# Optimization experiments

Measured on AMD Instinct MI355X. Metric: run time of the kernel, lower is better.

## Reference

```python
import jax, jax.numpy as jnp
import numpy as np

N_NODES = 100000
N_EDGES = 3200000
N_FEAT = 128
H = 16
N_CLASSES = 10


def gcn_conv(x, edge_index, W, b, num_nodes):
    """PyG GCNConv (eval): add self-loops, symmetric norm, linear, scatter-add, bias."""
    xw = x @ W  # [N, out]
    loops = jnp.arange(num_nodes, dtype=edge_index.dtype)
    src = jnp.concatenate([edge_index[0], loops])  # message sources (x_j)
    dst = jnp.concatenate([edge_index[1], loops])  # aggregation targets
    ones = jnp.ones(src.shape[0], dtype=xw.dtype)
    deg = jax.ops.segment_sum(ones, dst, num_segments=num_nodes)
    dinv = jnp.where(deg > 0, jax.lax.rsqrt(deg), 0.0)
    norm = dinv[src] * dinv[dst]  # [E+N]
    msg = xw[src] * norm[:, None]  # gather + scale
    out = jax.ops.segment_sum(msg, dst, num_segments=num_nodes)
    return out + b


def setup_inputs() -> dict:
    key = jax.random.key(0)
    ks = jax.random.split(key, 8)
    x = jax.random.normal(ks[0], (N_NODES, N_FEAT), dtype=jnp.float32)
    edge_index = jax.random.randint(ks[1], (2, N_EDGES), 0, N_NODES, dtype=jnp.int64)
    topo_edges = jax.random.randint(ks[2], (2, N_EDGES), 0, N_NODES, dtype=jnp.int64)
    s1 = 1.0 / np.sqrt(N_FEAT)
    s4 = 1.0 / np.sqrt(2 * H)
    W1 = jax.random.normal(ks[3], (N_FEAT, H), dtype=jnp.float32) * s1
    b1 = jnp.zeros((H,), dtype=jnp.float32)
    W2 = jax.random.normal(ks[4], (N_FEAT, H), dtype=jnp.float32) * s1
    b2 = jnp.zeros((H,), dtype=jnp.float32)
    W4 = jax.random.normal(ks[5], (2 * H, N_CLASSES), dtype=jnp.float32) * s4
    b4 = jnp.zeros((N_CLASSES,), dtype=jnp.float32)
    return {"x": x, "edge_index": edge_index, "topo_edges": topo_edges,
            "W1": W1, "b1": b1, "W2": W2, "b2": b2, "W4": W4, "b4": b4}


def reference(x, edge_index, topo_edges, W1, b1, W2, b2, W4, b4):
    n = x.shape[0]
    # branch 1: structural edges
    x1 = jax.nn.relu(gcn_conv(x, edge_index, W1, b1, n))
    # branch 2: topological edges
    x2 = jax.nn.relu(gcn_conv(x, topo_edges, W2, b2, n))
    # dropout is identity in eval mode
    h = jnp.concatenate([x1, x2], axis=1)  # [N, 2H]
    logits = gcn_conv(h, edge_index, W4, b4, n)  # [N, num_classes]
    return jax.nn.log_softmax(logits, axis=1)
```

## Files before the change

### kernel.cpp

```cpp
#include <hip/hip_runtime.h>
#include <hip/hip_fp16.h>

#define N_NODES 100000
#define N_EDGES 3200000
#define NB 1024
#define BW 98
#define SLOT 4096


__global__ void k_zero(int* __restrict__ bcur1, int* __restrict__ bcur2) {
    int i = blockIdx.x * blockDim.x + threadIdx.x;
    if (i < NB) { bcur1[i] = 0; bcur2[i] = 0; }
}

__global__ __launch_bounds__(256) void k_part(const int* __restrict__ ei, const int* __restrict__ te,
                                              int* __restrict__ bcur1, int* __restrict__ bcur2,
                                              unsigned* __restrict__ tmp1, unsigned* __restrict__ tmp2,
                                              int E, int PB) {
    __shared__ int h[NB];
    __shared__ int bas[NB];
    int gb = blockIdx.x;
    bool g2 = gb >= PB;
    const int* ed = g2 ? te : ei;
    int* bcur     = g2 ? bcur2 : bcur1;
    unsigned* tmp = g2 ? tmp2 : tmp1;
    int blk = g2 ? gb - PB : gb;
    int t = threadIdx.x;
    for (int i = t; i < NB; i += 256) h[i] = 0;
    __syncthreads();
    int base = blk * 8192, end = min(base + 8192, E);
    for (int e = base + t; e < end; e += 256) atomicAdd(&h[ed[E + e] / BW], 1);
    __syncthreads();
    for (int i = t; i < NB; i += 256) {
        int c = h[i];
        bas[i] = c ? atomicAdd(&bcur[i], c) : 0;
    }
    __syncthreads();
    for (int i = t; i < NB; i += 256) h[i] = 0;
    __syncthreads();
    for (int e = base + t; e < end; e += 256) {
        int d = ed[E + e], s = ed[e];
        int b = d / BW;
        int r = bas[b] + atomicAdd(&h[b], 1);
        if (r < SLOT) tmp[(size_t)b * SLOT + r] = ((unsigned)(d - b * BW) << 20) | (unsigned)s;
    }
}

__global__ __launch_bounds__(256) void k_csr(const int* __restrict__ bcur1, const int* __restrict__ bcur2,
                                             unsigned* __restrict__ tmp1, unsigned* __restrict__ tmp2,
                                             int2* __restrict__ pk1, int2* __restrict__ pk2,
                                             float* __restrict__ dinv1, float* __restrict__ dinv2, int n) {
    __shared__ unsigned stage[SLOT];
    __shared__ int ncnt[BW], noff[BW], nrank[BW];
    int gb = blockIdx.x;
    bool g2 = gb >= NB;
    int b = g2 ? gb - NB : gb;
    unsigned* tmp = g2 ? tmp2 : tmp1;
    int2* pk      = g2 ? pk2 : pk1;
    float* dinv   = g2 ? dinv2 : dinv1;
    int sz = min((g2 ? bcur2 : bcur1)[b], SLOT);
    int t = threadIdx.x;
    if (t < BW) { ncnt[t] = 0; nrank[t] = 0; }
    __syncthreads();
    size_t base = (size_t)b * SLOT;
    for (int i = t; i < sz; i += 256) {
        unsigned v = tmp[base + i];
        stage[i] = v;
        atomicAdd(&ncnt[v >> 20], 1);
    }
    __syncthreads();
    if (t == 0) {
        int run = 0;
        for (int k = 0; k < BW; ++k) { noff[k] = run; run += ncnt[k]; }
    }
    __syncthreads();
    int nd = b * BW + t;
    if (t < BW && nd < n) {
        pk[nd] = make_int2((int)base + noff[t], ncnt[t]);
        dinv[nd] = rsqrtf((float)ncnt[t] + 1.f);
    }
    for (int i = t; i < sz; i += 256) {
        unsigned v = stage[i];
        int ld = v >> 20;
        int r = atomicAdd(&nrank[ld], 1);
        tmp[base + noff[ld] + r] = v & 0xFFFFFu;
    }
}

__global__ __launch_bounds__(256) void k_gemm12(
    const float* __restrict__ x,
    const float* __restrict__ W1, const float* __restrict__ W2,
    const float* __restrict__ dinv1, const float* __restrict__ dinv2,
    __half* __restrict__ xwh1, __half* __restrict__ xwh2, int n) {
    __shared__ float Wl[128][32];
    __shared__ float xs[8][128];
    int t = threadIdx.x;
    for (int i = t; i < 128 * 16; i += 256) {
        int k = i / 16, o = i % 16;
        Wl[k][o]      = W1[i];
        Wl[k][o + 16] = W2[i];
    }
    int node0 = blockIdx.x * 8;
    for (int i = t; i < 8 * 128; i += 256) {
        int r = i >> 7, c = i & 127;
        int node = node0 + r;
        xs[r][c] = (node < n) ? x[node * 128 + c] : 0.f;
    }
    __syncthreads();
    int r = t >> 5, o = t & 31;
    int node = node0 + r;
    if (node < n) {
        float s = 0.f;
        #pragma unroll
        for (int k = 0; k < 128; ++k) s += xs[r][k] * Wl[k][o];
        if (o < 16) xwh1[(size_t)node * 16 + o]        = __float2half(s * dinv1[node]);
        else        xwh2[(size_t)node * 16 + (o - 16)] = __float2half(s * dinv2[node]);
    }
}

__global__ __launch_bounds__(256) void k_gather12(
    const __half* __restrict__ xwh1, const __half* __restrict__ xwh2,
    const unsigned* __restrict__ csr1, const unsigned* __restrict__ csr2,
    const int2* __restrict__ pk1, const int2* __restrict__ pk2,
    const float* __restrict__ dinv1, const float* __restrict__ dinv2,
    const float* __restrict__ b1, const float* __restrict__ b2,
    __half* __restrict__ h, int n) {
    int t = threadIdx.x;
    int node = blockIdx.x * 8 + (t >> 5);
    int c = t & 31;
    if (node >= n) return;
    bool g1 = (c < 16);
    int cl = g1 ? c : (c - 16);
    const __half* xw    = g1 ? xwh1 : xwh2;
    const unsigned* csr = g1 ? csr1 : csr2;
    int2 oc = g1 ? pk1[node] : pk2[node];
    int o = oc.x, m = oc.y;
    float di = g1 ? dinv1[node] : dinv2[node];
    float acc = __half2float(xw[(size_t)node * 16 + cl]);
    int k = 0;
    for (; k + 4 <= m; k += 4) {
        unsigned j0 = csr[o + k], j1 = csr[o + k + 1], j2 = csr[o + k + 2], j3 = csr[o + k + 3];
        acc += __half2float(xw[(size_t)j0 * 16 + cl]);
        acc += __half2float(xw[(size_t)j1 * 16 + cl]);
        acc += __half2float(xw[(size_t)j2 * 16 + cl]);
        acc += __half2float(xw[(size_t)j3 * 16 + cl]);
    }
    for (; k < m; ++k) acc += __half2float(xw[(size_t)csr[o + k] * 16 + cl]);
    acc *= di;
    float bv = g1 ? b1[cl] : b2[cl];
    float v = acc + bv;
    h[(size_t)node * 32 + c] = __float2half(v > 0.f ? v : 0.f);
}

__global__ void k_gemm3(const __half* __restrict__ h, const float* __restrict__ W4,
                        const float* __restrict__ dinv1, __half* __restrict__ zsh, int n) {
    int i = blockIdx.x * blockDim.x + threadIdx.x;
    if (i >= n) return;
    float hr[32];
    const __half2* hp = (const __half2*)(h + (size_t)i * 32);
    #pragma unroll
    for (int q = 0; q < 16; ++q) {
        float2 f = __half22float2(hp[q]);
        hr[2 * q] = f.x; hr[2 * q + 1] = f.y;
    }
    float di = dinv1[i];
    #pragma unroll
    for (int c = 0; c < 10; ++c) {
        float s = 0.f;
        #pragma unroll
        for (int k = 0; k < 32; ++k) s += hr[k] * W4[k * 10 + c];
        zsh[(size_t)i * 16 + c] = __float2half(s * di);
    }
}

__global__ __launch_bounds__(256) void k_gather3(
    const __half* __restrict__ zsh,
    const unsigned* __restrict__ csr1, const int2* __restrict__ pk1,
    const float* __restrict__ dinv1,
    const float* __restrict__ b4, float* __restrict__ out, int n) {
    int t = threadIdx.x;
    int node = blockIdx.x * 16 + (t >> 4);
    int c = t & 15;
    if (node >= n) return;
    bool act = (c < 10);
    int cc = act ? c : 0;
    float di = dinv1[node];
    float acc = __half2float(zsh[(size_t)node * 16 + cc]);
    int2 oc = pk1[node];
    int o = oc.x, m = oc.y;
    int k = 0;
    for (; k + 4 <= m; k += 4) {
        unsigned j0 = csr1[o + k], j1 = csr1[o + k + 1], j2 = csr1[o + k + 2], j3 = csr1[o + k + 3];
        acc += __half2float(zsh[(size_t)j0 * 16 + cc]);
        acc += __half2float(zsh[(size_t)j1 * 16 + cc]);
        acc += __half2float(zsh[(size_t)j2 * 16 + cc]);
        acc += __half2float(zsh[(size_t)j3 * 16 + cc]);
    }
    for (; k < m; ++k) acc += __half2float(zsh[(size_t)csr1[o + k] * 16 + cc]);
    float logit = acc * di + b4[cc];
    float mv = act ? logit : -1e30f;
    #pragma unroll
    for (int w = 8; w >= 1; w >>= 1) mv = fmaxf(mv, __shfl_xor(mv, w, 16));
    float ex = act ? expf(logit - mv) : 0.f;
    float ssum = ex;
    #pragma unroll
    for (int w = 8; w >= 1; w >>= 1) ssum += __shfl_xor(ssum, w, 16);
    if (act) out[(size_t)node * 10 + c] = logit - mv - logf(ssum);
}

extern "C" void kernel_launch(void* const* d_in, const int* in_sizes, int n_in,
                              void* d_out, int out_size, void* d_ws, size_t ws_size,
                              hipStream_t stream) {
    const float* x  = (const float*)d_in[0];
    const int*   ei = (const int*)d_in[1];
    const int*   te = (const int*)d_in[2];
    const float* W1 = (const float*)d_in[3];
    const float* b1 = (const float*)d_in[4];
    const float* W2 = (const float*)d_in[5];
    const float* b2 = (const float*)d_in[6];
    const float* W4 = (const float*)d_in[7];
    const float* b4 = (const float*)d_in[8];
    float* out = (float*)d_out;

    const int N = N_NODES, E = N_EDGES;

    char* w = (char*)d_ws;
    auto alloc = [&](size_t bytes) { void* p = (void*)w; w += (bytes + 255) & ~255ull; return p; };
    int*      bcur1 = (int*)alloc((size_t)NB * 4);
    int*      bcur2 = (int*)alloc((size_t)NB * 4);
    int2*     pk1   = (int2*)alloc((size_t)N * 8);
    int2*     pk2   = (int2*)alloc((size_t)N * 8);
    float*    dinv1 = (float*)alloc((size_t)N * 4);
    float*    dinv2 = (float*)alloc((size_t)N * 4);
    unsigned* tmp1  = (unsigned*)alloc((size_t)NB * SLOT * 4);
    unsigned* tmp2  = (unsigned*)alloc((size_t)NB * SLOT * 4);
    __half*   xwh1  = (__half*)alloc((size_t)N * 16 * 2);
    __half*   xwh2  = (__half*)alloc((size_t)N * 16 * 2);
    __half*   h     = (__half*)alloc((size_t)N * 32 * 2);
    __half*   zsh   = (__half*)alloc((size_t)N * 16 * 2);

    const int PB = (E + 8191) / 8192;
    k_zero<<<(NB + 255) / 256, 256, 0, stream>>>(bcur1, bcur2);
    k_part<<<2 * PB, 256, 0, stream>>>(ei, te, bcur1, bcur2, tmp1, tmp2, E, PB);
    k_csr<<<2 * NB, 256, 0, stream>>>(bcur1, bcur2, tmp1, tmp2, pk1, pk2, dinv1, dinv2, N);
    k_gemm12<<<(N + 7) / 8, 256, 0, stream>>>(x, W1, W2, dinv1, dinv2, xwh1, xwh2, N);
    k_gather12<<<(N + 7) / 8, 256, 0, stream>>>(xwh1, xwh2, tmp1, tmp2, pk1, pk2,
                                                dinv1, dinv2, b1, b2, h, N);
    k_gemm3<<<(N + 255) / 256, 256, 0, stream>>>(h, W4, dinv1, zsh, N);
    k_gather3<<<(N + 15) / 16, 256, 0, stream>>>(zsh, tmp1, pk1, dinv1, b4, out, N);
}
```

Measured before the change: 461.5 us.

## Locally sort edge chunk in LDS before scattering to bucket slots

The partition kernel now counting-sorts each chunk of edges by destination bucket in shared memory, using a block-wide prefix scan, and then writes them to global bucket slots in sorted order. Consecutive threads therefore write to contiguous addresses instead of scattering randomly. The chunk size doubles to 16384 edges per block, so each block needs about 77 KB of dynamic LDS. In exchange there are fewer blocks and lower occupancy, and every output element pays for a binary search over the bucket offsets.

```diff
diff --git a/kernel.cpp b/kernel.cpp
--- a/kernel.cpp
+++ b/kernel.cpp
@@ -6,6 +6,7 @@
 #define NB 1024
 #define BW 98
 #define SLOT 4096
+#define CHUNK 16384
 
 
 __global__ void k_zero(int* __restrict__ bcur1, int* __restrict__ bcur2) {
@@ -17,8 +18,13 @@
                                               int* __restrict__ bcur1, int* __restrict__ bcur2,
                                               unsigned* __restrict__ tmp1, unsigned* __restrict__ tmp2,
                                               int E, int PB) {
-    __shared__ int h[NB];
-    __shared__ int bas[NB];
+    extern __shared__ unsigned smem[];
+    unsigned* sorted = smem;
+    int* loff = (int*)(smem + CHUNK);
+    int* rank = loff + NB;
+    int* bas  = rank + NB;
+    int* ps   = bas + NB;
+
     int gb = blockIdx.x;
     bool g2 = gb >= PB;
     const int* ed = g2 ? te : ei;
@@ -26,23 +32,52 @@
     unsigned* tmp = g2 ? tmp2 : tmp1;
     int blk = g2 ? gb - PB : gb;
     int t = threadIdx.x;
-    for (int i = t; i < NB; i += 256) h[i] = 0;
-    __syncthreads();
-    int base = blk * 8192, end = min(base + 8192, E);
-    for (int e = base + t; e < end; e += 256) atomicAdd(&h[ed[E + e] / BW], 1);
-    __syncthreads();
-    for (int i = t; i < NB; i += 256) {
-        int c = h[i];
-        bas[i] = c ? atomicAdd(&bcur[i], c) : 0;
-    }
-    __syncthreads();
-    for (int i = t; i < NB; i += 256) h[i] = 0;
+
+    for (int i = t; i < NB; i += 256) rank[i] = 0;
+    __syncthreads();
+    int base = blk * CHUNK, end = min(base + CHUNK, E);
+    int csize = end - base;
+    for (int e = base + t; e < end; e += 256) atomicAdd(&rank[ed[E + e] / BW], 1);
+    __syncthreads();
+    int i4 = t * 4;
+    int c0 = rank[i4], c1 = rank[i4 + 1], c2 = rank[i4 + 2], c3 = rank[i4 + 3];
+    int tot = c0 + c1 + c2 + c3;
+    ps[t] = tot;
+    __syncthreads();
+    #pragma unroll
+    for (int d = 1; d < 256; d <<= 1) {
+        int a = (t >= d) ? ps[t - d] : 0;
+        __syncthreads();
+        ps[t] += a;
+        __syncthreads();
+    }
+    int excl = ps[t] - tot;
+    loff[i4]     = excl;
+    loff[i4 + 1] = excl + c0;
+    loff[i4 + 2] = excl + c0 + c1;
+    loff[i4 + 3] = excl + c0 + c1 + c2;
+    bas[i4]     = c0 ? atomicAdd(&bcur[i4], c0)     : 0;
+    bas[i4 + 1] = c1 ? atomicAdd(&bcur[i4 + 1], c1) : 0;
+    bas[i4 + 2] = c2 ? atomicAdd(&bcur[i4 + 2], c2) : 0;
+    bas[i4 + 3] = c3 ? atomicAdd(&bcur[i4 + 3], c3) : 0;
+    rank[i4] = 0; rank[i4 + 1] = 0; rank[i4 + 2] = 0; rank[i4 + 3] = 0;
     __syncthreads();
     for (int e = base + t; e < end; e += 256) {
         int d = ed[E + e], s = ed[e];
         int b = d / BW;
-        int r = bas[b] + atomicAdd(&h[b], 1);
-        if (r < SLOT) tmp[(size_t)b * SLOT + r] = ((unsigned)(d - b * BW) << 20) | (unsigned)s;
+        int r = atomicAdd(&rank[b], 1);
+        sorted[loff[b] + r] = ((unsigned)(d - b * BW) << 20) | (unsigned)s;
+    }
+    __syncthreads();
+    for (int i = t; i < csize; i += 256) {
+        int lo = 0, hi = NB - 1;
+        while (lo < hi) {
+            int mid = (lo + hi + 1) >> 1;
+            if (loff[mid] <= i) lo = mid; else hi = mid - 1;
+        }
+        int b = lo;
+        int pos = bas[b] + (i - loff[b]);
+        if (pos < SLOT) tmp[(size_t)b * SLOT + pos] = sorted[i];
     }
 }
 
@@ -239,9 +274,10 @@
     __half*   h     = (__half*)alloc((size_t)N * 32 * 2);
     __half*   zsh   = (__half*)alloc((size_t)N * 16 * 2);
 
-    const int PB = (E + 8191) / 8192;
+    const int PB = (E + CHUNK - 1) / CHUNK;
+    const size_t PART_LDS = ((size_t)CHUNK + 3 * NB + 256) * 4;
     k_zero<<<(NB + 255) / 256, 256, 0, stream>>>(bcur1, bcur2);
-    k_part<<<2 * PB, 256, 0, stream>>>(ei, te, bcur1, bcur2, tmp1, tmp2, E, PB);
+    k_part<<<2 * PB, 256, PART_LDS, stream>>>(ei, te, bcur1, bcur2, tmp1, tmp2, E, PB);
     k_csr<<<2 * NB, 256, 0, stream>>>(bcur1, bcur2, tmp1, tmp2, pk1, pk2, dinv1, dinv2, N);
     k_gemm12<<<(N + 7) / 8, 256, 0, stream>>>(x, W1, W2, dinv1, dinv2, xwh1, xwh2, N);
     k_gather12<<<(N + 7) / 8, 256, 0, stream>>>(xwh1, xwh2, tmp1, tmp2, pk1, pk2,
```

Result: faster. 426.0 us (-7.7%).
